# Performance work log

Hardware: AMD Instinct MI355X
Metric: run time of the kernel (lower is better)

Reference implementation:

```python
import jax, jax.numpy as jnp
import numpy as np

S, B, D, H, HD = 2048, 4, 1280, 16, 80  # seq, batch, d_model, heads, head_dim
NSEG = 8


def setup_inputs() -> dict:
    key = jax.random.key(0)
    k0, k1, k2 = jax.random.split(key, 3)
    x = jax.random.normal(k0, (S, B, D), dtype=jnp.float32)
    Wqkv = jax.random.normal(k1, (D, 3 * D), dtype=jnp.float32) * 0.02
    bqkv = jnp.zeros((3 * D,), dtype=jnp.float32)
    Wproj = jax.random.normal(k2, (D, 4 * D), dtype=jnp.float32) * 0.02
    bproj = jnp.zeros((4 * D,), dtype=jnp.float32)
    # 8 equal windows of 256 tokens: [0, 256, 512, ..., 2048]
    cu_seqlens = (jnp.arange(NSEG + 1, dtype=jnp.int32) * (S // NSEG))
    return {"x": x, "Wqkv": Wqkv, "bqkv": bqkv, "Wproj": Wproj,
            "bproj": bproj, "cu_seqlens": cu_seqlens}


def reference(x, Wqkv, bqkv, Wproj, bproj, cu_seqlens):
    s, b, d = x.shape
    qkv = x @ Wqkv + bqkv                     # [s, b, 3d]
    q, k, v = jnp.split(qkv, 3, axis=2)       # each [s, b, d]
    def to_bhsd(t):
        return t.reshape(s, b, H, HD).transpose(1, 2, 0, 3)  # [b, h, s, hd]
    q, k, v = to_bhsd(q), to_bhsd(k), to_bhsd(v)
    # Block-diagonal mask: token t belongs to window searchsorted(cu[1:], t, right)
    pos = jnp.arange(s)
    seg = jnp.searchsorted(cu_seqlens[1:], pos, side='right')  # [s]
    bias = jnp.where(seg[:, None] == seg[None, :], 0.0,
                     jnp.finfo(x.dtype).min)                   # [s, s]
    scale = 1.0 / jnp.sqrt(jnp.asarray(HD, dtype=x.dtype))
    scores = jnp.einsum('bhsd,bhtd->bhst', q, k) * scale + bias
    attn = jax.nn.softmax(scores, axis=-1)
    out = jnp.einsum('bhst,bhtd->bhsd', attn, v)               # [b, h, s, hd]
    context = out.transpose(2, 0, 1, 3).reshape(s, b, H * HD)  # [s, b, d]
    return context @ Wproj + bproj                             # [s, b, 4d]
```

## Files before the change

kernel.cpp:

```cpp
#include <hip/hip_runtime.h>

typedef _Float16 f16;
typedef _Float16 f16x8 __attribute__((ext_vector_type(8)));
typedef _Float16 f16x4 __attribute__((ext_vector_type(4)));
typedef float    f32x4 __attribute__((ext_vector_type(4)));
typedef unsigned int u32t;

#define AS1 __attribute__((address_space(1)))
#define AS3 __attribute__((address_space(3)))

static __device__ __forceinline__ void gload_lds16(const void* g, void* l) {
  __builtin_amdgcn_global_load_lds((const AS1 u32t*)g, (AS3 u32t*)l, 16, 0, 0);
}

static __device__ __forceinline__ f16x8 zero8() {
  f16x8 z;
#pragma unroll
  for (int j = 0; j < 8; ++j) z[j] = (f16)0;
  return z;
}

__global__ void k_cvt_x(const float* __restrict__ in, f16* __restrict__ out, int n4) {
  int stride = gridDim.x * blockDim.x;
  for (int i = blockIdx.x * blockDim.x + threadIdx.x; i < n4; i += stride) {
    float4 v = ((const float4*)in)[i];
    f16x4 o;
    o[0] = (f16)v.x; o[1] = (f16)v.y; o[2] = (f16)v.z; o[3] = (f16)v.w;
    ((f16x4*)out)[i] = o;
  }
}

__global__ void k_cvt_w_t(const float* __restrict__ W, f16* __restrict__ Wt, int N) {
  __shared__ float T[32][33];
  int bk = blockIdx.x % 40;
  int bn = blockIdx.x / 40;
  int k0 = bk * 32, n0 = bn * 32;
  int r = threadIdx.x >> 5;
  int c = threadIdx.x & 31;
#pragma unroll
  for (int i = 0; i < 4; ++i)
    T[r + i * 8][c] = W[(size_t)(k0 + r + i * 8) * N + n0 + c];
  __syncthreads();
#pragma unroll
  for (int i = 0; i < 4; ++i)
    Wt[(size_t)(n0 + r + i * 8) * 1280 + k0 + c] = (f16)T[c][r + i * 8];
}


template<int NCOLS, bool F16OUT>
__global__ __launch_bounds__(512, 2)
void gemm_nt(const f16* __restrict__ A, const f16* __restrict__ Bt,
             const float* __restrict__ bias, void* __restrict__ Cout)
{
  __shared__ __align__(16) char lds[131072];
  const int tid = threadIdx.x;
  const int wave = tid >> 6, lane = tid & 63;
  const int rl = lane & 15, g = lane >> 4;
  const int wm = wave >> 2, wn = wave & 3;

  constexpr int NBN = NCOLS / 256;
  constexpr int NWG = 32 * NBN;
  const int bid = blockIdx.x;
  const int wgid = (bid & 7) * (NWG / 8) + (bid >> 3);
  const int bm = wgid / NBN, bn = wgid % NBN;
  const long row0 = (long)bm * 256, col0 = (long)bn * 256;

  const int srow = tid >> 3;
  const int scol = ((tid & 7) ^ (srow & 7)) << 4;
  const char* gA = (const char*)A  + (row0 + srow) * 2560 + scol;
  const char* gB = (const char*)Bt + (col0 + srow) * 2560 + scol;
  char* const ldsw = lds + wave * 1024;

  auto STAGE = [&](int isB, int buf, int half, int kb) {
    const char* s = (isB ? gB : gA) + half * (128 * 2560) + kb;
    char* d = ldsw + isB * 65536 + buf * 32768 + half * 16384;
    gload_lds16(s, d);
    gload_lds16(s + 64 * 2560, d + 8192);
  };

  const int swz0 = ((0 + g) ^ (rl & 7)) << 4;
  const int swz1 = ((4 + g) ^ (rl & 7)) << 4;
  const int aoff = (wm * 128 + rl) << 7;
  const int boff = 65536 + ((wn * 64 + rl) << 7);

  auto LDA = [&](f16x8 (&af)[8], int buf, int mh) {
#pragma unroll
    for (int m = 0; m < 4; ++m) {
      const char* p = lds + buf * 32768 + aoff + (mh * 4 + m) * 2048;
      af[m * 2 + 0] = *(const f16x8*)(p + swz0);
      af[m * 2 + 1] = *(const f16x8*)(p + swz1);
    }
  };
  auto LDB = [&](f16x8 (&bf)[4], int buf, int nh) {
#pragma unroll
    for (int n = 0; n < 2; ++n) {
      const char* p = lds + buf * 32768 + boff + (nh * 2 + n) * 2048;
      bf[n * 2 + 0] = *(const f16x8*)(p + swz0);
      bf[n * 2 + 1] = *(const f16x8*)(p + swz1);
    }
  };

  f32x4 acc[8][4];
#pragma unroll
  for (int m = 0; m < 8; ++m)
#pragma unroll
    for (int n = 0; n < 4; ++n) acc[m][n] = (f32x4){0.f, 0.f, 0.f, 0.f};

  auto MM = [&](int mh, int nh, const f16x8 (&af)[8], const f16x8 (&bf)[4]) {
    __builtin_amdgcn_s_setprio(1);
#pragma unroll
    for (int m = 0; m < 4; ++m)
#pragma unroll
      for (int n = 0; n < 2; ++n)
#pragma unroll
        for (int kk = 0; kk < 2; ++kk)
          acc[mh * 4 + m][nh * 2 + n] = __builtin_amdgcn_mfma_f32_16x16x32_f16(
              af[m * 2 + kk], bf[n * 2 + kk], acc[mh * 4 + m][nh * 2 + n], 0, 0, 0);
    __builtin_amdgcn_s_setprio(0);
  };

#define BAR()    __builtin_amdgcn_s_barrier()
#define WLGKM()  asm volatile("s_waitcnt lgkmcnt(0)" ::: "memory")
#define WVM(N)   asm volatile("s_waitcnt vmcnt(" #N ")" ::: "memory")

  auto TILE = [&](int buf,
                  int s0b, int s0u, int s0h, int s0k,
                  int s1b, int s1u, int s1h, int s1k,
                  int s2b, int s2u, int s2h, int s2k,
                  int s3b, int s3u, int s3h, int s3k,
                  int vmend, bool endbar) {
    f16x8 af[8], bf0[4], bf1[4];
    LDA(af, buf, 0); LDB(bf0, buf, 0);
    if (s0k >= 0) STAGE(s0b, s0u, s0h, s0k);
    BAR(); WLGKM(); MM(0, 0, af, bf0); BAR();
    LDB(bf1, buf, 1);
    if (s1k >= 0) STAGE(s1b, s1u, s1h, s1k);
    BAR(); WLGKM(); MM(0, 1, af, bf1); BAR();
    LDA(af, buf, 1);
    if (s2k >= 0) STAGE(s2b, s2u, s2h, s2k);
    BAR(); WLGKM(); MM(1, 1, af, bf1); BAR();
    if (s3k >= 0) STAGE(s3b, s3u, s3h, s3k);
    BAR(); MM(1, 0, af, bf0);
    if (vmend == 2) WVM(2);
    else if (vmend == 0) WVM(0);
    if (endbar) BAR();
  };

  STAGE(0, 0, 0, 0); STAGE(0, 0, 1, 0); STAGE(1, 0, 0, 0); STAGE(1, 0, 1, 0);
  STAGE(0, 1, 0, 128);
  WVM(2); BAR();

#pragma unroll 1
  for (int it = 0; it < 9; ++it) {
    const int kb = it * 256;
    TILE(0,
         0, 1, 1, kb + 128,
         1, 1, 0, kb + 128,
         1, 1, 1, kb + 128,
         0, 0, 0, kb + 256,
         2, true);
    TILE(1,
         0, 0, 1, kb + 256,
         1, 0, 0, kb + 256,
         1, 0, 1, kb + 256,
         0, 1, 0, kb + 384,
         2, true);
  }
  TILE(0,
       0, 1, 1, 2432,
       1, 1, 0, 2432,
       1, 1, 1, 2432,
       0, 0, 0, -1,
       0, true);
  TILE(1, 0,0,0,-1, 0,0,0,-1, 0,0,0,-1, 0,0,0,-1, -1, false);

#undef BAR
#undef WLGKM
#undef WVM

#pragma unroll
  for (int m = 0; m < 8; ++m) {
#pragma unroll
    for (int n = 0; n < 4; ++n) {
      long c = col0 + wn * 64 + n * 16 + rl;
      float bv = bias[c];
#pragma unroll
      for (int r = 0; r < 4; ++r) {
        long rr = row0 + wm * 128 + m * 16 + g * 4 + r;
        float v = acc[m][n][r] + bv;
        if (F16OUT) ((f16*)Cout)[rr * NCOLS + c] = (f16)v;
        else        ((float*)Cout)[rr * NCOLS + c] = v;
      }
    }
  }
}

__global__ void k_vt(const f16* __restrict__ qkv, f16* __restrict__ vt) {
  __shared__ __align__(16) f16 T[128 * 136];
  int bid = blockIdx.x;
  int sc16 = bid & 15, bh = bid >> 4;
  int b = bh >> 4, h = bh & 15;
  int s0 = sc16 * 128;
  int t = threadIdx.x;
#pragma unroll
  for (int i = 0; i < 5; ++i) {
    int cid = i * 256 + t;
    int s = cid / 10, c = cid % 10;
    const f16* g = qkv + (size_t)((s0 + s) * 4 + b) * 3840 + 2560 + h * 80 + c * 8;
    f16x8 v = *(const f16x8*)g;
    int phys = c ^ ((s >> 3) & 7);
    *(f16x8*)(T + s * 136 + phys * 8) = v;
  }
  __syncthreads();
#pragma unroll
  for (int i = 0; i < 5; ++i) {
    int oid = i * 256 + t;
    int sc8 = oid & 15, hd = oid >> 4;
    f16x8 o;
#pragma unroll
    for (int j = 0; j < 8; ++j) {
      int row = sc8 * 8 + j;
      int phys = (hd >> 3) ^ (sc8 & 7);
      o[j] = T[row * 136 + phys * 8 + (hd & 7)];
    }
    *(f16x8*)(vt + (size_t)(bh * 80 + hd) * 2048 + s0 + sc8 * 8) = o;
  }
}

__global__ __launch_bounds__(512, 2)
void k_attn(const f16* __restrict__ qkv, const f16* __restrict__ vt,
            f16* __restrict__ ctx)
{
  __shared__ __align__(16) f16 sK[256 * 104];
  __shared__ __align__(16) f16 sV[80 * 264];
  __shared__ __align__(16) f16 sP[128 * 72];

  const int bid = blockIdx.x;
  const int qc = bid & 1, seg = (bid >> 1) & 7, h = (bid >> 4) & 15, b = bid >> 8;
  const int t = threadIdx.x;
  const int wave = t >> 6, lane = t & 63;
  const int s_key0 = seg * 256;

#pragma unroll
  for (int i = 0; i < 5; ++i) {
    int cid = i * 512 + t;
    int key = cid / 10, c = cid % 10;
    const f16* g = qkv + (size_t)((s_key0 + key) * 4 + b) * 3840 + 1280 + h * 80 + c * 8;
    *(f16x8*)(sK + key * 104 + c * 8) = *(const f16x8*)g;
  }
  {
    int key = t >> 1, c = t & 1;
    *(f16x8*)(sK + key * 104 + 80 + c * 8) = zero8();
  }
#pragma unroll
  for (int i = 0; i < 5; ++i) {
    int cid = i * 512 + t;
    int hd = cid >> 5, c = cid & 31;
    const f16* g = vt + (size_t)((b * 16 + h) * 80 + hd) * 2048 + s_key0 + c * 8;
    *(f16x8*)(sV + hd * 264 + c * 8) = *(const f16x8*)g;
  }

  const int q0 = s_key0 + qc * 128 + wave * 16;
  const int rl = lane & 15, g = lane >> 4;
  f16x8 qf[3];
  {
    const f16* gq = qkv + (size_t)((q0 + rl) * 4 + b) * 3840 + h * 80;
    qf[0] = *(const f16x8*)(gq + g * 8);
    qf[1] = *(const f16x8*)(gq + 32 + g * 8);
    if (g < 2) qf[2] = *(const f16x8*)(gq + 64 + g * 8);
    else       qf[2] = zero8();
  }
  __syncthreads();

  f32x4 sc[16];
#pragma unroll
  for (int nt = 0; nt < 16; ++nt) sc[nt] = (f32x4){0.f, 0.f, 0.f, 0.f};
#pragma unroll
  for (int nt = 0; nt < 16; ++nt) {
#pragma unroll
    for (int kk = 0; kk < 3; ++kk) {
      f16x8 bf = *(const f16x8*)(sK + (nt * 16 + rl) * 104 + kk * 32 + g * 8);
      sc[nt] = __builtin_amdgcn_mfma_f32_16x16x32_f16(qf[kk], bf, sc[nt], 0, 0, 0);
    }
  }

  const float scale = 0.11180339887498949f;
  float inv[4];
#pragma unroll
  for (int r = 0; r < 4; ++r) {
    float m = -1e30f;
#pragma unroll
    for (int nt = 0; nt < 16; ++nt) m = fmaxf(m, sc[nt][r]);
#pragma unroll
    for (int off = 8; off >= 1; off >>= 1) m = fmaxf(m, __shfl_xor(m, off));
    m *= scale;
    float sum = 0.f;
#pragma unroll
    for (int nt = 0; nt < 16; ++nt) {
      float p = __expf(sc[nt][r] * scale - m);
      sc[nt][r] = p;
      sum += p;
    }
#pragma unroll
    for (int off = 8; off >= 1; off >>= 1) sum += __shfl_xor(sum, off);
    inv[r] = 1.0f / sum;
  }

  f32x4 o[5];
#pragma unroll
  for (int nt = 0; nt < 5; ++nt) o[nt] = (f32x4){0.f, 0.f, 0.f, 0.f};
  const int prow0 = wave * 16;
  for (int ch = 0; ch < 4; ++ch) {
    __syncthreads();
#pragma unroll
    for (int f = 0; f < 4; ++f) {
      int nt = ch * 4 + f;
#pragma unroll
      for (int r = 0; r < 4; ++r)
        sP[(prow0 + g * 4 + r) * 72 + f * 16 + rl] = (f16)sc[nt][r];
    }
    __syncthreads();
#pragma unroll
    for (int kk = 0; kk < 2; ++kk) {
      f16x8 pa = *(const f16x8*)(sP + (prow0 + rl) * 72 + kk * 32 + g * 8);
#pragma unroll
      for (int nt = 0; nt < 5; ++nt) {
        f16x8 vb = *(const f16x8*)(sV + (nt * 16 + rl) * 264 + ch * 64 + kk * 32 + g * 8);
        o[nt] = __builtin_amdgcn_mfma_f32_16x16x32_f16(pa, vb, o[nt], 0, 0, 0);
      }
    }
  }

#pragma unroll
  for (int nt = 0; nt < 5; ++nt) {
    int hd = nt * 16 + rl;
#pragma unroll
    for (int r = 0; r < 4; ++r) {
      long qrow = q0 + g * 4 + r;
      float v = o[nt][r] * inv[r];
      ctx[(qrow * 4 + b) * 1280 + h * 80 + hd] = (f16)v;
    }
  }
}

extern "C" void kernel_launch(void* const* d_in, const int* in_sizes, int n_in,
                              void* d_out, int out_size, void* d_ws, size_t ws_size,
                              hipStream_t stream)
{
  const float* x     = (const float*)d_in[0];
  const float* Wqkv  = (const float*)d_in[1];
  const float* bqkv  = (const float*)d_in[2];
  const float* Wproj = (const float*)d_in[3];
  const float* bproj = (const float*)d_in[4];

  char* ws = (char*)d_ws;
  f16* X16   = (f16*)(ws);
  f16* WQT   = (f16*)(ws + 20971520);
  f16* WPT   = (f16*)(ws + 30801920);
  f16* QKV16 = (f16*)(ws + 43909120);
  f16* VT    = (f16*)(ws + 106823680);
  f16* CTX16 = X16;

  k_cvt_x<<<4096, 256, 0, stream>>>(x, X16, 8192 * 1280 / 4);
  k_cvt_w_t<<<40 * 120, 256, 0, stream>>>(Wqkv, WQT, 3840);
  k_cvt_w_t<<<40 * 160, 256, 0, stream>>>(Wproj, WPT, 5120);
  gemm_nt<3840, true ><<<480, 512, 0, stream>>>(X16, WQT, bqkv, QKV16);
  k_vt<<<1024, 256, 0, stream>>>(QKV16, VT);
  k_attn<<<1024, 512, 0, stream>>>(QKV16, VT, CTX16);
  gemm_nt<5120, false><<<640, 512, 0, stream>>>(CTX16, WPT, bproj, d_out);
}
```

Baseline: 281.5 us.

## Simplify GEMM pipeline to whole-tile double buffering and drop attention P barriers

Replaces the hand-scheduled GEMM main loop with a plain double-buffered loop. Each iteration issues the next full 128-K tile of A and B into the other LDS buffer, runs all MFMAs on the current buffer, then synchronises once, removing the interleaved stage/barrier/waitcnt choreography. The LDS layout changes to 64KB per buffer holding A and B together. Separately, it removes the two __syncthreads around the per-wave P staging in attention, since each wave only writes and reads its own 16 rows. The cost is coarser overlap of loads with MFMAs, and it depends on __syncthreads draining the async LDS loads correctly.

Result: no change. 281.6 us (+0.0%).

```diff
diff --git a/kernel.cpp b/kernel.cpp
--- a/kernel.cpp
+++ b/kernel.cpp
@@ -71,22 +71,30 @@
   const char* gB = (const char*)Bt + (col0 + srow) * 2560 + scol;
   char* const ldsw = lds + wave * 1024;
 
-  auto STAGE = [&](int isB, int buf, int half, int kb) {
-    const char* s = (isB ? gB : gA) + half * (128 * 2560) + kb;
-    char* d = ldsw + isB * 65536 + buf * 32768 + half * 16384;
-    gload_lds16(s, d);
-    gload_lds16(s + 64 * 2560, d + 8192);
+  auto STAGE4 = [&](int tk, int buf) {
+    const long kb = (long)tk * 128;
+#pragma unroll
+    for (int half = 0; half < 2; ++half) {
+      const char* sa = gA + half * (128 * 2560) + kb;
+      char* da = ldsw + buf * 65536 + half * 16384;
+      gload_lds16(sa, da);
+      gload_lds16(sa + 64 * 2560, da + 8192);
+      const char* sb = gB + half * (128 * 2560) + kb;
+      char* db = ldsw + buf * 65536 + 32768 + half * 16384;
+      gload_lds16(sb, db);
+      gload_lds16(sb + 64 * 2560, db + 8192);
+    }
   };
 
   const int swz0 = ((0 + g) ^ (rl & 7)) << 4;
   const int swz1 = ((4 + g) ^ (rl & 7)) << 4;
   const int aoff = (wm * 128 + rl) << 7;
-  const int boff = 65536 + ((wn * 64 + rl) << 7);
+  const int boff = 32768 + ((wn * 64 + rl) << 7);
 
   auto LDA = [&](f16x8 (&af)[8], int buf, int mh) {
 #pragma unroll
     for (int m = 0; m < 4; ++m) {
-      const char* p = lds + buf * 32768 + aoff + (mh * 4 + m) * 2048;
+      const char* p = lds + buf * 65536 + aoff + (mh * 4 + m) * 2048;
       af[m * 2 + 0] = *(const f16x8*)(p + swz0);
       af[m * 2 + 1] = *(const f16x8*)(p + swz1);
     }
@@ -94,7 +102,7 @@
   auto LDB = [&](f16x8 (&bf)[4], int buf, int nh) {
 #pragma unroll
     for (int n = 0; n < 2; ++n) {
-      const char* p = lds + buf * 32768 + boff + (nh * 2 + n) * 2048;
+      const char* p = lds + buf * 65536 + boff + (nh * 2 + n) * 2048;
       bf[n * 2 + 0] = *(const f16x8*)(p + swz0);
       bf[n * 2 + 1] = *(const f16x8*)(p + swz1);
     }
@@ -119,64 +127,29 @@
     __builtin_amdgcn_s_setprio(0);
   };
 
-#define BAR()    __builtin_amdgcn_s_barrier()
-#define WLGKM()  asm volatile("s_waitcnt lgkmcnt(0)" ::: "memory")
-#define WVM(N)   asm volatile("s_waitcnt vmcnt(" #N ")" ::: "memory")
-
-  auto TILE = [&](int buf,
-                  int s0b, int s0u, int s0h, int s0k,
-                  int s1b, int s1u, int s1h, int s1k,
-                  int s2b, int s2u, int s2h, int s2k,
-                  int s3b, int s3u, int s3h, int s3k,
-                  int vmend, bool endbar) {
-    f16x8 af[8], bf0[4], bf1[4];
-    LDA(af, buf, 0); LDB(bf0, buf, 0);
-    if (s0k >= 0) STAGE(s0b, s0u, s0h, s0k);
-    BAR(); WLGKM(); MM(0, 0, af, bf0); BAR();
+  auto TILEBODY = [&](int buf, int stk) {
+    if (stk >= 0) STAGE4(stk, buf ^ 1);
+    f16x8 afL[8], afH[8], bf0[4], bf1[4];
+    LDA(afL, buf, 0);
+    LDB(bf0, buf, 0);
     LDB(bf1, buf, 1);
-    if (s1k >= 0) STAGE(s1b, s1u, s1h, s1k);
-    BAR(); WLGKM(); MM(0, 1, af, bf1); BAR();
-    LDA(af, buf, 1);
-    if (s2k >= 0) STAGE(s2b, s2u, s2h, s2k);
-    BAR(); WLGKM(); MM(1, 1, af, bf1); BAR();
-    if (s3k >= 0) STAGE(s3b, s3u, s3h, s3k);
-    BAR(); MM(1, 0, af, bf0);
-    if (vmend == 2) WVM(2);
-    else if (vmend == 0) WVM(0);
-    if (endbar) BAR();
-  };
-
-  STAGE(0, 0, 0, 0); STAGE(0, 0, 1, 0); STAGE(1, 0, 0, 0); STAGE(1, 0, 1, 0);
-  STAGE(0, 1, 0, 128);
-  WVM(2); BAR();
+    MM(0, 0, afL, bf0);
+    MM(0, 1, afL, bf1);
+    LDA(afH, buf, 1);
+    MM(1, 1, afH, bf1);
+    MM(1, 0, afH, bf0);
+  };
+
+  STAGE4(0, 0);
+  __syncthreads();
 
 #pragma unroll 1
-  for (int it = 0; it < 9; ++it) {
-    const int kb = it * 256;
-    TILE(0,
-         0, 1, 1, kb + 128,
-         1, 1, 0, kb + 128,
-         1, 1, 1, kb + 128,
-         0, 0, 0, kb + 256,
-         2, true);
-    TILE(1,
-         0, 0, 1, kb + 256,
-         1, 0, 0, kb + 256,
-         1, 0, 1, kb + 256,
-         0, 1, 0, kb + 384,
-         2, true);
-  }
-  TILE(0,
-       0, 1, 1, 2432,
-       1, 1, 0, 2432,
-       1, 1, 1, 2432,
-       0, 0, 0, -1,
-       0, true);
-  TILE(1, 0,0,0,-1, 0,0,0,-1, 0,0,0,-1, 0,0,0,-1, -1, false);
-
-#undef BAR
-#undef WLGKM
-#undef WVM
+  for (int tp = 0; tp < 10; ++tp) {
+    TILEBODY(0, 2 * tp + 1);
+    __syncthreads();
+    TILEBODY(1, tp < 9 ? 2 * tp + 2 : -1);
+    __syncthreads();
+  }
 
 #pragma unroll
   for (int m = 0; m < 8; ++m) {
@@ -311,7 +284,6 @@
   for (int nt = 0; nt < 5; ++nt) o[nt] = (f32x4){0.f, 0.f, 0.f, 0.f};
   const int prow0 = wave * 16;
   for (int ch = 0; ch < 4; ++ch) {
-    __syncthreads();
 #pragma unroll
     for (int f = 0; f < 4; ++f) {
       int nt = ch * 4 + f;
@@ -319,7 +291,6 @@
       for (int r = 0; r < 4; ++r)
         sP[(prow0 + g * 4 + r) * 72 + f * 16 + rl] = (f16)sc[nt][r];
     }
-    __syncthreads();
 #pragma unroll
     for (int kk = 0; kk < 2; ++kk) {
       f16x8 pa = *(const f16x8*)(sP + (prow0 + rl) * 72 + kk * 32 + g * 8);
```
